# Optimization experiments

Measured on AMD Instinct MI355X. Metric: run time of the kernel, lower is better.

The kernel has to match this reference:

```python
import jax, jax.numpy as jnp
import numpy as np

H = 8           # attention heads
SPARSITY = 0.5  # fraction of keys kept per query row

def _silu(x):
    return x * jax.nn.sigmoid(x)

def _forward(x_t, t, te_w1, te_b1, te_w2, te_b2, fe_w1, fe_b1, fe_w2, fe_b2,
             fp_w1, fp_b1, fp_w2, fp_b2, fp_w3, fp_b3, fid_emb,
             wq, bq, wk, bk, wv, bv, wo, bo,
             gp_w1, gp_b1, gp_w2, gp_b2, ln_g, ln_b,
             dn_w1, dn_b1, dn_w2, dn_b2, dn_w3, dn_b3):
    B, F = x_t.shape
    D = te_w1.shape[1]
    hd = D // H
    # time / feature embeddings (Linear-SiLU-Linear)
    t_emb = _silu(t[:, None] @ te_w1 + te_b1) @ te_w2 + te_b2        # [B, D]
    x_emb = _silu(x_t @ fe_w1 + fe_b1) @ fe_w2 + fe_b2               # [B, D]
    comb = jnp.concatenate([
        jnp.broadcast_to(x_emb[:, None, :], (B, F, D)),
        jnp.broadcast_to(t_emb[:, None, :], (B, F, D))], axis=-1)    # [B, F, 2D]
    # shared per-feature processor (n_features > 32 branch)
    h = _silu(comb @ fp_w1 + fp_b1)
    h = _silu(h @ fp_w2 + fp_b2)
    h = h @ fp_w3 + fp_b3                                            # [B, F, D]
    d4 = fid_emb.shape[1]
    fid_pad = jnp.concatenate([fid_emb, jnp.zeros((F, D - d4), h.dtype)], axis=-1)
    feats = h + 0.1 * fid_pad[None]                                  # [B, F, D]
    # sparse feature attention (dropout is identity in eval)
    def split(x):
        return x.reshape(B, F, H, hd).transpose(0, 2, 1, 3)          # [B, H, F, hd]
    q = split(feats @ wq + bq)
    k = split(feats @ wk + bk)
    v = split(feats @ wv + bv)
    scores = jnp.einsum('bhqd,bhkd->bhqk', q, k) / (hd ** 0.5)
    k_value = max(1, int(F * SPARSITY))
    thr = jax.lax.top_k(scores, k_value)[0][..., -1:]                # kth largest per row
    scores = jnp.where(scores < thr, -1e9, scores)                   # masked_fill(-1e9)
    attn = jax.nn.softmax(scores, axis=-1)
    out = jnp.einsum('bhqk,bhkd->bhqd', attn, v)
    out = out.transpose(0, 2, 1, 3).reshape(B, F, D) @ wo + bo       # [B, F, D]
    # global pooling + processor with LayerNorm (eps=1e-5)
    g = out.mean(axis=1)
    g = _silu(g @ gp_w1 + gp_b1) @ gp_w2 + gp_b2
    mu = g.mean(-1, keepdims=True)
    var = ((g - mu) ** 2).mean(-1, keepdims=True)
    g = (g - mu) / jnp.sqrt(var + 1e-5) * ln_g + ln_b
    # denoise net -> tanh of mean half
    r = _silu(g @ dn_w1 + dn_b1)
    r = _silu(r @ dn_w2 + dn_b2)
    r = r @ dn_w3 + dn_b3                                            # [B, 2F]
    return jnp.tanh(r[:, :F])

def setup_inputs():
    B, F, D = 512, 128, 512
    D4 = D // 4
    ks = iter(jax.random.split(jax.random.key(0), 40))
    def w(shape):
        return jax.random.normal(next(ks), shape, jnp.float32) / np.sqrt(shape[0]).astype(np.float32)
    z = lambda n: jnp.zeros((n,), jnp.float32)
    return dict(
        x_t=jax.random.normal(next(ks), (B, F), jnp.float32),
        t=jax.random.uniform(next(ks), (B,), jnp.float32),
        te_w1=w((1, D)), te_b1=z(D), te_w2=w((D, D)), te_b2=z(D),
        fe_w1=w((F, D)), fe_b1=z(D), fe_w2=w((D, D)), fe_b2=z(D),
        fp_w1=w((2 * D, D)), fp_b1=z(D), fp_w2=w((D, D)), fp_b2=z(D),
        fp_w3=w((D, D)), fp_b3=z(D),
        fid_emb=jax.random.normal(next(ks), (F, D4), jnp.float32),
        wq=w((D, D)), bq=z(D), wk=w((D, D)), bk=z(D),
        wv=w((D, D)), bv=z(D), wo=w((D, D)), bo=z(D),
        gp_w1=w((D, 2 * D)), gp_b1=z(2 * D), gp_w2=w((2 * D, D)), gp_b2=z(D),
        ln_g=jnp.ones((D,), jnp.float32), ln_b=z(D),
        dn_w1=w((D, 2 * D)), dn_b1=z(2 * D), dn_w2=w((2 * D, 2 * D)), dn_b2=z(2 * D),
        dn_w3=w((2 * D, 2 * F)), dn_b3=z(2 * F),
    )

def reference(x_t, t, te_w1, te_b1, te_w2, te_b2, fe_w1, fe_b1, fe_w2, fe_b2,
              fp_w1, fp_b1, fp_w2, fp_b2, fp_w3, fp_b3, fid_emb,
              wq, bq, wk, bk, wv, bv, wo, bo,
              gp_w1, gp_b1, gp_w2, gp_b2, ln_g, ln_b,
              dn_w1, dn_b1, dn_w2, dn_b2, dn_w3, dn_b3):
    return _forward(x_t, t, te_w1, te_b1, te_w2, te_b2, fe_w1, fe_b1, fe_w2, fe_b2,
                    fp_w1, fp_b1, fp_w2, fp_b2, fp_w3, fp_b3, fid_emb,
                    wq, bq, wk, bk, wv, bv, wo, bo,
                    gp_w1, gp_b1, gp_w2, gp_b2, ln_g, ln_b,
                    dn_w1, dn_b1, dn_w2, dn_b2, dn_w3, dn_b3)
```

## Files before the change

kernel.cpp:

```cpp
#include <hip/hip_runtime.h>

__device__ __forceinline__ float silu_f(float x) { return x / (1.f + __expf(-x)); }

struct AOp {
  const float* P;
  const float* w1;
  const float* b0;
  int lda;
  int tgen;
};

template <int NPROB, int T1GEN>
__global__ __launch_bounds__(256) void gemm_p(
    AOp a0, AOp a1,
    const float* __restrict__ B0, const float* __restrict__ B1,
    const float* __restrict__ B2, int ldb,
    float* __restrict__ O0, float* __restrict__ O1, float* __restrict__ O2,
    int ldc, int Kslab, int ls, long slabMN) {
  __shared__ float As[2][32][68];
  __shared__ float Bs[2][32][68];
  const int tid = threadIdx.x;
  const int z = blockIdx.z;
  const int zi = (NPROB > 1) ? (z >> ls) : 0;
  const int s  = (NPROB > 1) ? (z & ((1 << ls) - 1)) : z;
  const AOp a = (NPROB > 1 && zi == 1) ? a1 : a0;
  const float* Bp = ((NPROB > 2 && zi == 2) ? B2 : (zi == 1) ? B1 : B0)
                    + (long)(s * Kslab) * ldb;
  float* Obase = ((NPROB > 2 && zi == 2) ? O2 : (zi == 1) ? O1 : O0)
                 + (long)s * slabMN;
  const int kbase = s * Kslab;
  const long bm = blockIdx.y * 64, bn = blockIdx.x * 64;
  const int tg = T1GEN ? a.tgen : 0;

  float acc[4][4] = {};
  const int ar = tid >> 3;
  const int ak = (tid & 7) << 2;
  const int br = tid >> 4;
  const int bn4 = (tid & 15) << 2;
  const int ty = tid >> 4, tx = tid & 15;

  float4 rA[2];
  float4 rB[2];
  float4 rW, rC;
  float tm0 = 0.f, tm1 = 0.f;

  auto loadA = [&](int k0) {
    int kg = kbase + k0 + ak;
    if (T1GEN && tg) {
      rW = *(const float4*)&a.w1[kg];
      rC = *(const float4*)&a.b0[kg];
    } else {
#pragma unroll
      for (int h = 0; h < 2; ++h)
        rA[h] = *(const float4*)&a.P[(bm + ar + h * 32) * (long)a.lda + kg];
    }
  };
  auto loadB = [&](int k0) {
#pragma unroll
    for (int h = 0; h < 2; ++h)
      rB[h] = *(const float4*)&Bp[(long)(k0 + br + h * 16) * ldb + bn + bn4];
  };
  auto store = [&](int buf) {
#pragma unroll
    for (int h = 0; h < 2; ++h) {
      int m = ar + h * 32;
      float4 av;
      if (T1GEN && tg) {
        float tm = h ? tm1 : tm0;
        av.x = silu_f(tm * rW.x + rC.x);
        av.y = silu_f(tm * rW.y + rC.y);
        av.z = silu_f(tm * rW.z + rC.z);
        av.w = silu_f(tm * rW.w + rC.w);
      } else {
        av = rA[h];
      }
      As[buf][ak + 0][m] = av.x; As[buf][ak + 1][m] = av.y;
      As[buf][ak + 2][m] = av.z; As[buf][ak + 3][m] = av.w;
    }
#pragma unroll
    for (int h = 0; h < 2; ++h) *(float4*)&Bs[buf][br + h * 16][bn4] = rB[h];
  };

  if (T1GEN && tg) { tm0 = a.P[bm + ar]; tm1 = a.P[bm + ar + 32]; }
  loadA(0); loadB(0);
  store(0);
  if (32 < Kslab) { loadA(32); loadB(32); }

  int cur = 0;
  for (int k0 = 0; k0 < Kslab; k0 += 32) {
    __syncthreads();
    if (k0 + 32 < Kslab) store(cur ^ 1);
    if (k0 + 64 < Kslab) { loadA(k0 + 64); loadB(k0 + 64); }
#pragma unroll
    for (int k = 0; k < 32; ++k) {
      float4 a4 = *(const float4*)&As[cur][k][ty << 2];
      float4 b4 = *(const float4*)&Bs[cur][k][tx << 2];
      float am[4] = {a4.x, a4.y, a4.z, a4.w};
      float bv[4] = {b4.x, b4.y, b4.z, b4.w};
#pragma unroll
      for (int i = 0; i < 4; ++i)
#pragma unroll
        for (int j = 0; j < 4; ++j) acc[i][j] = fmaf(am[i], bv[j], acc[i][j]);
    }
    cur ^= 1;
  }

  float* O = Obase + (bm + ty * 4) * (long)ldc + bn + tx * 4;
#pragma unroll
  for (int i = 0; i < 4; ++i) {
    float4 v = {acc[i][0], acc[i][1], acc[i][2], acc[i][3]};
    *(float4*)&O[(long)i * ldc] = v;
  }
}

__global__ __launch_bounds__(256) void gemm_bt(
    const float* __restrict__ A, int lda, const float* __restrict__ B, int ldb,
    float* __restrict__ OUT, int ldc, int K, float alpha,
    int zAoff, int zBoff, int zCoff) {
  __shared__ float As[2][32][68];
  __shared__ float Bs[2][32][68];
  const int tid = threadIdx.x;
  const int z = blockIdx.z;
  const long bm = blockIdx.y * 64, bn = blockIdx.x * 64;
  const float* Ab = A + (long)z * zAoff;
  const float* Bp = B + (long)z * zBoff;
  float* Obase = OUT + (long)z * zCoff;
  float acc[4][4] = {};
  const int ar = tid >> 3;
  const int ak = (tid & 7) << 2;
  const int ty = tid >> 4, tx = tid & 15;
  float4 rA[2], rB[2];
  auto loadAB = [&](int k0) {
#pragma unroll
    for (int h = 0; h < 2; ++h) {
      rA[h] = *(const float4*)&Ab[(bm + ar + h * 32) * (long)lda + k0 + ak];
      rB[h] = *(const float4*)&Bp[(bn + ar + h * 32) * (long)ldb + k0 + ak];
    }
  };
  auto store = [&](int buf) {
#pragma unroll
    for (int h = 0; h < 2; ++h) {
      int m = ar + h * 32;
      As[buf][ak + 0][m] = rA[h].x; As[buf][ak + 1][m] = rA[h].y;
      As[buf][ak + 2][m] = rA[h].z; As[buf][ak + 3][m] = rA[h].w;
      Bs[buf][ak + 0][m] = rB[h].x; Bs[buf][ak + 1][m] = rB[h].y;
      Bs[buf][ak + 2][m] = rB[h].z; Bs[buf][ak + 3][m] = rB[h].w;
    }
  };
  loadAB(0); store(0);
  if (32 < K) loadAB(32);
  int cur = 0;
  for (int k0 = 0; k0 < K; k0 += 32) {
    __syncthreads();
    if (k0 + 32 < K) store(cur ^ 1);
    if (k0 + 64 < K) loadAB(k0 + 64);
#pragma unroll
    for (int k = 0; k < 32; ++k) {
      float4 a4 = *(const float4*)&As[cur][k][ty << 2];
      float4 b4 = *(const float4*)&Bs[cur][k][tx << 2];
      float am[4] = {a4.x, a4.y, a4.z, a4.w};
      float bv[4] = {b4.x, b4.y, b4.z, b4.w};
#pragma unroll
      for (int i = 0; i < 4; ++i)
#pragma unroll
        for (int j = 0; j < 4; ++j) acc[i][j] = fmaf(am[i], bv[j], acc[i][j]);
    }
    cur ^= 1;
  }
  float* O = Obase + (bm + ty * 4) * (long)ldc + bn + tx * 4;
#pragma unroll
  for (int i = 0; i < 4; ++i) {
    float4 v = {alpha * acc[i][0], alpha * acc[i][1], alpha * acc[i][2],
                alpha * acc[i][3]};
    *(float4*)&O[(long)i * ldc] = v;
  }
}

template <int NS, int ACT>
__global__ __launch_bounds__(256) void sumk(
    const float* __restrict__ P, long slabMN,
    const float* __restrict__ b0, const float* __restrict__ b1, int bsplit,
    int cmask, float* __restrict__ out) {
  int i4 = (blockIdx.x * 256 + threadIdx.x) << 2;
  float4 s = *(const float4*)&P[i4];
#pragma unroll
  for (int si = 1; si < NS; ++si) {
    float4 p = *(const float4*)&P[(long)si * slabMN + i4];
    s.x += p.x; s.y += p.y; s.z += p.z; s.w += p.w;
  }
  int c = i4 & cmask;
  const float* bp = (b1 && c >= bsplit) ? (b1 + c - bsplit) : (b0 + c);
  float4 bb = *(const float4*)bp;
  s.x += bb.x; s.y += bb.y; s.z += bb.z; s.w += bb.w;
  if (ACT == 1) {
    s.x = silu_f(s.x); s.y = silu_f(s.y); s.z = silu_f(s.z); s.w = silu_f(s.w);
  }
  *(float4*)&out[i4] = s;
}

__global__ __launch_bounds__(256) void reduce_tanh(
    const float* __restrict__ P, int slabMN, int nslab,
    const float* __restrict__ bias, float* __restrict__ C) {
  int i4 = (blockIdx.x * 256 + threadIdx.x) << 2;
  float4 s = *(const float4*)&P[i4];
  for (int si = 1; si < nslab; ++si) {
    float4 p = *(const float4*)&P[(long)si * slabMN + i4];
    s.x += p.x; s.y += p.y; s.z += p.z; s.w += p.w;
  }
  int c = i4 & 127;
  float4 v = {tanhf(s.x + bias[c]), tanhf(s.y + bias[c + 1]),
              tanhf(s.z + bias[c + 2]), tanhf(s.w + bias[c + 3])};
  *(float4*)&C[i4] = v;
}

__global__ __launch_bounds__(256) void attn_kernel(
    const float* __restrict__ PBq,
    const float* __restrict__ bq,
    const float* __restrict__ bv,
    const float* __restrict__ kf,
    const float* __restrict__ Mm,
    const float* __restrict__ vf,
    float* __restrict__ pool) {
  const int b = blockIdx.x, h = blockIdx.y;
  const int tid = threadIdx.x;
  __shared__ float uq[64];
  __shared__ float uls[128];
  __shared__ float wpart[4][128];
  __shared__ float wcol[128];
  __shared__ float ppart[2][64];

  if (tid < 64) {
    int c = h * 64 + tid;
    long o = (long)b * 512 + c;
    uq[tid] = PBq[o] + PBq[262144 + o] + PBq[524288 + o] + PBq[786432 + o] + bq[c];
  }
  __syncthreads();
  if (tid < 128) {
    const float* kr = kf + (long)tid * 512 + h * 64;
    float acc = 0.f;
#pragma unroll
    for (int d4 = 0; d4 < 16; ++d4) {
      float4 kv = *(const float4*)&kr[d4 * 4];
      acc += uq[d4 * 4] * kv.x + uq[d4 * 4 + 1] * kv.y +
             uq[d4 * 4 + 2] * kv.z + uq[d4 * 4 + 3] * kv.w;
    }
    uls[tid] = 0.0125f * acc;
  }
  __syncthreads();

  const int lane = tid & 63;
  const int wave = tid >> 6;
  const float u0 = uls[lane], u1 = uls[lane + 64];

  float blo = -0.5f, bhi = 0.5f;
#pragma unroll
  for (int it = 0; it < 11; ++it) {
    float mid = 0.5f * (blo + bhi);
    int n = __popcll(__ballot(u0 >= mid)) + __popcll(__ballot(u1 >= mid));
    bool ge = (n >= 64);
    blo = ge ? mid : blo;
    bhi = ge ? bhi : mid;
  }
  const float wlo = blo - 0.014f, whi = blo + 0.014f;

  float wc0 = 0.f, wc1 = 0.f;
  const float* Mh = Mm + h * 128;
  const int i0 = wave * 32;
  float a0r = Mh[(long)i0 * 1024 + lane];
  float a1r = Mh[(long)i0 * 1024 + lane + 64];
  float b0r = Mh[(long)(i0 + 1) * 1024 + lane];
  float b1r = Mh[(long)(i0 + 1) * 1024 + lane + 64];
  for (int r = 0; r < 32; r += 2) {
    float TA0 = u0 + a0r, TA1 = u1 + a1r;
    float TB0 = u0 + b0r, TB1 = u1 + b1r;
    if (r < 30) {
      a0r = Mh[(long)(i0 + r + 2) * 1024 + lane];
      a1r = Mh[(long)(i0 + r + 2) * 1024 + lane + 64];
      b0r = Mh[(long)(i0 + r + 3) * 1024 + lane];
      b1r = Mh[(long)(i0 + r + 3) * 1024 + lane + 64];
    }
    float loA = wlo, hiA = whi, loB = wlo, hiB = whi;
#pragma unroll
    for (int it = 0; it < 5; ++it) {
      float midA = 0.5f * (loA + hiA), midB = 0.5f * (loB + hiB);
      int nA = __popcll(__ballot(TA0 >= midA)) + __popcll(__ballot(TA1 >= midA));
      int nB = __popcll(__ballot(TB0 >= midB)) + __popcll(__ballot(TB1 >= midB));
      bool gA = (nA >= 64), gB = (nB >= 64);
      loA = gA ? midA : loA; hiA = gA ? hiA : midA;
      loB = gB ? midB : loB; hiB = gB ? hiB : midB;
    }
    float pA0 = (TA0 >= loA) ? __expf(TA0 - loA) : 0.f;
    float pA1 = (TA1 >= loA) ? __expf(TA1 - loA) : 0.f;
    float pB0 = (TB0 >= loB) ? __expf(TB0 - loB) : 0.f;
    float pB1 = (TB1 >= loB) ? __expf(TB1 - loB) : 0.f;
    float sA = pA0 + pA1, sB = pB0 + pB1;
#pragma unroll
    for (int d = 1; d < 64; d <<= 1) {
      sA += __shfl_xor(sA, d);
      sB += __shfl_xor(sB, d);
    }
    float ivA = 1.f / sA, ivB = 1.f / sB;
    wc0 += pA0 * ivA + pB0 * ivB;
    wc1 += pA1 * ivA + pB1 * ivB;
  }
  wpart[wave][lane] = wc0;
  wpart[wave][lane + 64] = wc1;
  __syncthreads();
  if (tid < 128) {
    wcol[tid] = (wpart[0][tid] + wpart[1][tid] + wpart[2][tid] + wpart[3][tid]) *
                (1.f / 128.f);
  }
  __syncthreads();
  if (wave < 2) {
    int j0 = wave * 64;
    const float* vfp = vf + h * 64 + lane;
    float acc = 0.f;
#pragma unroll 8
    for (int jj = 0; jj < 64; ++jj) acc += wcol[j0 + jj] * vfp[(long)(j0 + jj) * 512];
    ppart[wave][lane] = acc;
  }
  __syncthreads();
  if (tid < 64) {
    int d = tid;
    int c = h * 64 + d;
    long o = (long)b * 512 + c;
    long vb0 = 4 * 262144;
    float v = PBq[vb0 + o] + PBq[vb0 + 262144 + o] + PBq[vb0 + 524288 + o] +
              PBq[vb0 + 786432 + o] + bv[c];
    pool[o] = 0.1f * (ppart[0][d] + ppart[1][d]) + v;
  }
}

template <int NSLAB>
__global__ __launch_bounds__(256) void ln_kernel(const float* __restrict__ P,
                                                 const float* __restrict__ bias,
                                                 const float* __restrict__ g,
                                                 const float* __restrict__ bb,
                                                 float* __restrict__ Y) {
  int row = blockIdx.x;
  int tid = threadIdx.x;
  long o0 = (long)row * 512 + tid;
  long o1 = o0 + 256;
  float v0 = bias[tid], v1 = bias[tid + 256];
#pragma unroll
  for (int s = 0; s < NSLAB; ++s) {
    v0 += P[(long)s * 262144 + o0];
    v1 += P[(long)s * 262144 + o1];
  }
  float s = v0 + v1;
#pragma unroll
  for (int d = 1; d < 64; d <<= 1) s += __shfl_xor(s, d);
  __shared__ float r1[4], r2[4];
  if ((tid & 63) == 0) r1[tid >> 6] = s;
  __syncthreads();
  float mean = (r1[0] + r1[1] + r1[2] + r1[3]) * (1.f / 512.f);
  float d0 = v0 - mean, d1 = v1 - mean;
  float q = d0 * d0 + d1 * d1;
#pragma unroll
  for (int d = 1; d < 64; d <<= 1) q += __shfl_xor(q, d);
  if ((tid & 63) == 0) r2[tid >> 6] = q;
  __syncthreads();
  float var = (r2[0] + r2[1] + r2[2] + r2[3]) * (1.f / 512.f);
  float inv = rsqrtf(var + 1e-5f);
  Y[(long)row * 512 + tid] = d0 * inv * g[tid] + bb[tid];
  Y[(long)row * 512 + tid + 256] = d1 * inv * g[tid + 256] + bb[tid + 256];
}


extern "C" void kernel_launch(void* const* d_in, const int* in_sizes, int n_in,
                              void* d_out, int out_size, void* d_ws, size_t ws_size,
                              hipStream_t stream) {
  const float* x_t = (const float*)d_in[0];
  const float* t_in = (const float*)d_in[1];
  const float* te_w1 = (const float*)d_in[2];
  const float* te_b1 = (const float*)d_in[3];
  const float* te_w2 = (const float*)d_in[4];
  const float* te_b2 = (const float*)d_in[5];
  const float* fe_w1 = (const float*)d_in[6];
  const float* fe_b1 = (const float*)d_in[7];
  const float* fe_w2 = (const float*)d_in[8];
  const float* fe_b2 = (const float*)d_in[9];
  const float* fp_w1 = (const float*)d_in[10];
  const float* fp_b1 = (const float*)d_in[11];
  const float* fp_w2 = (const float*)d_in[12];
  const float* fp_b2 = (const float*)d_in[13];
  const float* fp_w3 = (const float*)d_in[14];
  const float* fp_b3 = (const float*)d_in[15];
  const float* fid = (const float*)d_in[16];
  const float* wq = (const float*)d_in[17];
  const float* bq = (const float*)d_in[18];
  const float* wk = (const float*)d_in[19];
  const float* wv = (const float*)d_in[21];
  const float* bv = (const float*)d_in[22];
  const float* wo = (const float*)d_in[23];
  const float* bo = (const float*)d_in[24];
  const float* gp_w1 = (const float*)d_in[25];
  const float* gp_b1 = (const float*)d_in[26];
  const float* gp_w2 = (const float*)d_in[27];
  const float* gp_b2 = (const float*)d_in[28];
  const float* ln_g = (const float*)d_in[29];
  const float* ln_b = (const float*)d_in[30];
  const float* dn_w1 = (const float*)d_in[31];
  const float* dn_b1 = (const float*)d_in[32];
  const float* dn_w2 = (const float*)d_in[33];
  const float* dn_b2 = (const float*)d_in[34];
  const float* dn_w3 = (const float*)d_in[35];
  const float* dn_b3 = (const float*)d_in[36];

  float* W = (float*)d_ws;
  float* P  = W;
  float* XC = W + 2097152;
  float* SA = W + 2621440;
  float* SB = W + 2883584;
  float* qf = W + 3145728;
  float* kf = W + 3211264;
  float* vf = W + 3276800;
  float* Mb = W + 3342336;

  auto ap = [](const float* Pm, int lda) {
    AOp a; a.P = Pm; a.w1 = nullptr; a.b0 = nullptr; a.lda = lda; a.tgen = 0;
    return a;
  };

  gemm_p<3, 0><<<dim3(8, 2, 3), 256, 0, stream>>>(
      ap(fid, 128), ap(fid, 128), wq, wk, wv, 512, qf, kf, vf, 512, 128, 0, 0);
  gemm_bt<<<dim3(2, 2, 8), 256, 0, stream>>>(qf, 512, kf, 512, Mb, 1024, 64,
                                             0.00125f, 64, 64, 128);
  gemm_p<1, 0><<<dim3(8, 8, 4), 256, 0, stream>>>(
      ap(x_t, 128), ap(x_t, 128), fe_w1, nullptr, nullptr, 512,
      P, nullptr, nullptr, 512, 32, 0, 262144);
  sumk<4, 1><<<256, 256, 0, stream>>>(P, 262144, fe_b1, nullptr, 0, 511, SA);
  {
    AOp a1; a1.P = t_in; a1.w1 = te_w1; a1.b0 = te_b1; a1.lda = 0; a1.tgen = 1;
    gemm_p<2, 1><<<dim3(8, 8, 8), 256, 0, stream>>>(
        ap(SA, 512), a1, fe_w2, te_w2, nullptr, 512,
        P, P + 512, nullptr, 1024, 128, 2, 524288);
  }
  sumk<4, 0><<<512, 256, 0, stream>>>(P, 524288, fe_b2, te_b2, 512, 1023, XC);
  gemm_p<1, 0><<<dim3(8, 8, 8), 256, 0, stream>>>(
      ap(XC, 1024), ap(XC, 1024), fp_w1, nullptr, nullptr, 512,
      P, nullptr, nullptr, 512, 128, 0, 262144);
  sumk<8, 1><<<256, 256, 0, stream>>>(P, 262144, fp_b1, nullptr, 0, 511, SB);
  gemm_p<1, 0><<<dim3(8, 8, 8), 256, 0, stream>>>(
      ap(SB, 512), ap(SB, 512), fp_w2, nullptr, nullptr, 512,
      P, nullptr, nullptr, 512, 64, 0, 262144);
  sumk<8, 1><<<256, 256, 0, stream>>>(P, 262144, fp_b2, nullptr, 0, 511, SA);
  gemm_p<1, 0><<<dim3(8, 8, 8), 256, 0, stream>>>(
      ap(SA, 512), ap(SA, 512), fp_w3, nullptr, nullptr, 512,
      P, nullptr, nullptr, 512, 64, 0, 262144);
  sumk<8, 0><<<256, 256, 0, stream>>>(P, 262144, fp_b3, nullptr, 0, 511, SB);
  gemm_p<2, 0><<<dim3(8, 8, 8), 256, 0, stream>>>(
      ap(SB, 512), ap(SB, 512), wq, wv, nullptr, 512,
      P, P + 1048576, nullptr, 512, 128, 2, 262144);
  attn_kernel<<<dim3(512, 8), 256, 0, stream>>>(P, bq, bv, kf, Mb, vf, SA);
  gemm_p<1, 0><<<dim3(8, 8, 8), 256, 0, stream>>>(
      ap(SA, 512), ap(SA, 512), wo, nullptr, nullptr, 512,
      P, nullptr, nullptr, 512, 64, 0, 262144);
  sumk<8, 0><<<256, 256, 0, stream>>>(P, 262144, bo, nullptr, 0, 511, SB);
  gemm_p<1, 0><<<dim3(16, 8, 4), 256, 0, stream>>>(
      ap(SB, 512), ap(SB, 512), gp_w1, nullptr, nullptr, 1024,
      P, nullptr, nullptr, 1024, 128, 0, 524288);
  sumk<4, 1><<<512, 256, 0, stream>>>(P, 524288, gp_b1, nullptr, 0, 1023, XC);
  gemm_p<1, 0><<<dim3(8, 8, 8), 256, 0, stream>>>(
      ap(XC, 1024), ap(XC, 1024), gp_w2, nullptr, nullptr, 512,
      P, nullptr, nullptr, 512, 128, 0, 262144);
  ln_kernel<8><<<512, 256, 0, stream>>>(P, gp_b2, ln_g, ln_b, SA);
  gemm_p<1, 0><<<dim3(16, 8, 4), 256, 0, stream>>>(
      ap(SA, 512), ap(SA, 512), dn_w1, nullptr, nullptr, 1024,
      P, nullptr, nullptr, 1024, 128, 0, 524288);
  sumk<4, 1><<<512, 256, 0, stream>>>(P, 524288, dn_b1, nullptr, 0, 1023, XC);
  gemm_p<1, 0><<<dim3(16, 8, 4), 256, 0, stream>>>(
      ap(XC, 1024), ap(XC, 1024), dn_w2, nullptr, nullptr, 1024,
      P, nullptr, nullptr, 1024, 256, 0, 524288);
  sumk<4, 1><<<512, 256, 0, stream>>>(P, 524288, dn_b2, nullptr, 0, 1023, XC);
  gemm_p<1, 0><<<dim3(2, 8, 16), 256, 0, stream>>>(
      ap(XC, 1024), ap(XC, 1024), dn_w3, nullptr, nullptr, 256,
      P, nullptr, nullptr, 128, 64, 0, 65536);
  reduce_tanh<<<64, 256, 0, stream>>>(P, 65536, 16, dn_b3, (float*)d_out);
}
```

Baseline: 288.0 us.

## Fuse split-K reductions into GEMMs via atomic tile counters and prefold fp_w1 weights

Split-K partial sums are now reduced inside the GEMM kernel by the last-arriving block for each tile, tracked with an atomic counter, which replaces the separate sumk and reduce_tanh launches. The fe_w2/te_w2 products with fp_w1 are precomputed as weight-weight GEMMs, and a folded bias is built, so the concatenated 1024-wide embedding step collapses into one GEMM per branch. Several small prologue GEMMs (QKV of fid, QK^T mask, first feature layer) are merged into two multi-role kernels. This cuts launch count and intermediate traffic, at the cost of threadfence/atomic overhead, a memset, and some extra weight-weight GEMM work per call.

```diff
diff --git a/kernel.cpp b/kernel.cpp
--- a/kernel.cpp
+++ b/kernel.cpp
@@ -2,70 +2,50 @@
 
 __device__ __forceinline__ float silu_f(float x) { return x / (1.f + __expf(-x)); }
 
-struct AOp {
-  const float* P;
-  const float* w1;
-  const float* b0;
-  int lda;
-  int tgen;
-};
-
-template <int NPROB, int T1GEN>
-__global__ __launch_bounds__(256) void gemm_p(
-    AOp a0, AOp a1,
-    const float* __restrict__ B0, const float* __restrict__ B1,
-    const float* __restrict__ B2, int ldb,
-    float* __restrict__ O0, float* __restrict__ O1, float* __restrict__ O2,
-    int ldc, int Kslab, int ls, long slabMN) {
-  __shared__ float As[2][32][68];
-  __shared__ float Bs[2][32][68];
+template <int TG, int BT>
+__device__ __forceinline__ void dev_gemm(
+    float (*As)[32][68], float (*Bs)[32][68],
+    const float* __restrict__ Ap, int lda,
+    const float* __restrict__ tw1, const float* __restrict__ tb0,
+    const float* __restrict__ Bp, int ldb,
+    float* __restrict__ Obase, int ldc,
+    int kbase, int Kslab, long bm, long bn, float alpha) {
   const int tid = threadIdx.x;
-  const int z = blockIdx.z;
-  const int zi = (NPROB > 1) ? (z >> ls) : 0;
-  const int s  = (NPROB > 1) ? (z & ((1 << ls) - 1)) : z;
-  const AOp a = (NPROB > 1 && zi == 1) ? a1 : a0;
-  const float* Bp = ((NPROB > 2 && zi == 2) ? B2 : (zi == 1) ? B1 : B0)
-                    + (long)(s * Kslab) * ldb;
-  float* Obase = ((NPROB > 2 && zi == 2) ? O2 : (zi == 1) ? O1 : O0)
-                 + (long)s * slabMN;
-  const int kbase = s * Kslab;
-  const long bm = blockIdx.y * 64, bn = blockIdx.x * 64;
-  const int tg = T1GEN ? a.tgen : 0;
-
+  const int ar = tid >> 3, ak = (tid & 7) << 2;
+  const int br = tid >> 4, bn4 = (tid & 15) << 2;
+  const int ty = tid >> 4, tx = tid & 15;
   float acc[4][4] = {};
-  const int ar = tid >> 3;
-  const int ak = (tid & 7) << 2;
-  const int br = tid >> 4;
-  const int bn4 = (tid & 15) << 2;
-  const int ty = tid >> 4, tx = tid & 15;
-
-  float4 rA[2];
-  float4 rB[2];
-  float4 rW, rC;
+  float4 rA[2], rB[2], rW, rC;
   float tm0 = 0.f, tm1 = 0.f;
-
+  if (TG) { tm0 = Ap[bm + ar]; tm1 = Ap[bm + ar + 32]; }
   auto loadA = [&](int k0) {
     int kg = kbase + k0 + ak;
-    if (T1GEN && tg) {
-      rW = *(const float4*)&a.w1[kg];
-      rC = *(const float4*)&a.b0[kg];
+    if (TG) {
+      rW = *(const float4*)&tw1[kg];
+      rC = *(const float4*)&tb0[kg];
     } else {
 #pragma unroll
       for (int h = 0; h < 2; ++h)
-        rA[h] = *(const float4*)&a.P[(bm + ar + h * 32) * (long)a.lda + kg];
+        rA[h] = *(const float4*)&Ap[(bm + ar + h * 32) * (long)lda + kg];
     }
   };
   auto loadB = [&](int k0) {
-#pragma unroll
-    for (int h = 0; h < 2; ++h)
-      rB[h] = *(const float4*)&Bp[(long)(k0 + br + h * 16) * ldb + bn + bn4];
+    if (BT) {
+#pragma unroll
+      for (int h = 0; h < 2; ++h)
+        rB[h] = *(const float4*)&Bp[(bn + ar + h * 32) * (long)ldb + kbase + k0 + ak];
+    } else {
+#pragma unroll
+      for (int h = 0; h < 2; ++h)
+        rB[h] = *(const float4*)&Bp[(long)(k0 + br + h * 16) * ldb + bn + bn4];
+    }
   };
   auto store = [&](int buf) {
 #pragma unroll
     for (int h = 0; h < 2; ++h) {
       int m = ar + h * 32;
       float4 av;
-      if (T1GEN && tg) {
+      if (TG) {
         float tm = h ? tm1 : tm0;
         av.x = silu_f(tm * rW.x + rC.x);
         av.y = silu_f(tm * rW.y + rC.y);
@@ -77,15 +57,21 @@
       As[buf][ak + 0][m] = av.x; As[buf][ak + 1][m] = av.y;
       As[buf][ak + 2][m] = av.z; As[buf][ak + 3][m] = av.w;
     }
-#pragma unroll
-    for (int h = 0; h < 2; ++h) *(float4*)&Bs[buf][br + h * 16][bn4] = rB[h];
+    if (BT) {
+#pragma unroll
+      for (int h = 0; h < 2; ++h) {
+        int n = ar + h * 32;
+        Bs[buf][ak + 0][n] = rB[h].x; Bs[buf][ak + 1][n] = rB[h].y;
+        Bs[buf][ak + 2][n] = rB[h].z; Bs[buf][ak + 3][n] = rB[h].w;
+      }
+    } else {
+#pragma unroll
+      for (int h = 0; h < 2; ++h) *(float4*)&Bs[buf][br + h * 16][bn4] = rB[h];
+    }
   };
-
-  if (T1GEN && tg) { tm0 = a.P[bm + ar]; tm1 = a.P[bm + ar + 32]; }
   loadA(0); loadB(0);
   store(0);
   if (32 < Kslab) { loadA(32); loadB(32); }
-
   int cur = 0;
   for (int k0 = 0; k0 < Kslab; k0 += 32) {
     __syncthreads();
@@ -104,69 +90,6 @@
     }
     cur ^= 1;
   }
-
-  float* O = Obase + (bm + ty * 4) * (long)ldc + bn + tx * 4;
-#pragma unroll
-  for (int i = 0; i < 4; ++i) {
-    float4 v = {acc[i][0], acc[i][1], acc[i][2], acc[i][3]};
-    *(float4*)&O[(long)i * ldc] = v;
-  }
-}
-
-__global__ __launch_bounds__(256) void gemm_bt(
-    const float* __restrict__ A, int lda, const float* __restrict__ B, int ldb,
-    float* __restrict__ OUT, int ldc, int K, float alpha,
-    int zAoff, int zBoff, int zCoff) {
-  __shared__ float As[2][32][68];
-  __shared__ float Bs[2][32][68];
-  const int tid = threadIdx.x;
-  const int z = blockIdx.z;
-  const long bm = blockIdx.y * 64, bn = blockIdx.x * 64;
-  const float* Ab = A + (long)z * zAoff;
-  const float* Bp = B + (long)z * zBoff;
-  float* Obase = OUT + (long)z * zCoff;
-  float acc[4][4] = {};
-  const int ar = tid >> 3;
-  const int ak = (tid & 7) << 2;
-  const int ty = tid >> 4, tx = tid & 15;
-  float4 rA[2], rB[2];
-  auto loadAB = [&](int k0) {
-#pragma unroll
-    for (int h = 0; h < 2; ++h) {
-      rA[h] = *(const float4*)&Ab[(bm + ar + h * 32) * (long)lda + k0 + ak];
-      rB[h] = *(const float4*)&Bp[(bn + ar + h * 32) * (long)ldb + k0 + ak];
-    }
-  };
-  auto store = [&](int buf) {
-#pragma unroll
-    for (int h = 0; h < 2; ++h) {
-      int m = ar + h * 32;
-      As[buf][ak + 0][m] = rA[h].x; As[buf][ak + 1][m] = rA[h].y;
-      As[buf][ak + 2][m] = rA[h].z; As[buf][ak + 3][m] = rA[h].w;
-      Bs[buf][ak + 0][m] = rB[h].x; Bs[buf][ak + 1][m] = rB[h].y;
-      Bs[buf][ak + 2][m] = rB[h].z; Bs[buf][ak + 3][m] = rB[h].w;
-    }
-  };
-  loadAB(0); store(0);
-  if (32 < K) loadAB(32);
-  int cur = 0;
-  for (int k0 = 0; k0 < K; k0 += 32) {
-    __syncthreads();
-    if (k0 + 32 < K) store(cur ^ 1);
-    if (k0 + 64 < K) loadAB(k0 + 64);
-#pragma unroll
-    for (int k = 0; k < 32; ++k) {
-      float4 a4 = *(const float4*)&As[cur][k][ty << 2];
-      float4 b4 = *(const float4*)&Bs[cur][k][tx << 2];
-      float am[4] = {a4.x, a4.y, a4.z, a4.w};
-      float bv[4] = {b4.x, b4.y, b4.z, b4.w};
-#pragma unroll
-      for (int i = 0; i < 4; ++i)
-#pragma unroll
-        for (int j = 0; j < 4; ++j) acc[i][j] = fmaf(am[i], bv[j], acc[i][j]);
-    }
-    cur ^= 1;
-  }
   float* O = Obase + (bm + ty * 4) * (long)ldc + bn + tx * 4;
 #pragma unroll
   for (int i = 0; i < 4; ++i) {
@@ -176,50 +99,139 @@
   }
 }
 
-template <int NS, int ACT>
-__global__ __launch_bounds__(256) void sumk(
-    const float* __restrict__ P, long slabMN,
-    const float* __restrict__ b0, const float* __restrict__ b1, int bsplit,
-    int cmask, float* __restrict__ out) {
-  int i4 = (blockIdx.x * 256 + threadIdx.x) << 2;
-  float4 s = *(const float4*)&P[i4];
-#pragma unroll
-  for (int si = 1; si < NS; ++si) {
-    float4 p = *(const float4*)&P[(long)si * slabMN + i4];
-    s.x += p.x; s.y += p.y; s.z += p.z; s.w += p.w;
-  }
-  int c = i4 & cmask;
-  const float* bp = (b1 && c >= bsplit) ? (b1 + c - bsplit) : (b0 + c);
-  float4 bb = *(const float4*)bp;
-  s.x += bb.x; s.y += bb.y; s.z += bb.z; s.w += bb.w;
-  if (ACT == 1) {
-    s.x = silu_f(s.x); s.y = silu_f(s.y); s.z = silu_f(s.z); s.w = silu_f(s.w);
-  }
-  *(float4*)&out[i4] = s;
-}
-
-__global__ __launch_bounds__(256) void reduce_tanh(
-    const float* __restrict__ P, int slabMN, int nslab,
-    const float* __restrict__ bias, float* __restrict__ C) {
-  int i4 = (blockIdx.x * 256 + threadIdx.x) << 2;
-  float4 s = *(const float4*)&P[i4];
-  for (int si = 1; si < nslab; ++si) {
-    float4 p = *(const float4*)&P[(long)si * slabMN + i4];
-    s.x += p.x; s.y += p.y; s.z += p.z; s.w += p.w;
-  }
-  int c = i4 & 127;
-  float4 v = {tanhf(s.x + bias[c]), tanhf(s.y + bias[c + 1]),
-              tanhf(s.z + bias[c + 2]), tanhf(s.w + bias[c + 3])};
-  *(float4*)&C[i4] = v;
+template <int RACT>
+__device__ __forceinline__ void reduce_tile(
+    const float* __restrict__ Pb, long slabMN, int nslab,
+    const float* __restrict__ bias, float* __restrict__ cmp, int ldcmp,
+    long bm, long bn, int ldc) {
+  const int tid = threadIdx.x;
+  const int r0 = (tid >> 4) * 4, c0 = (tid & 15) * 4;
+  float4 bb = *(const float4*)&bias[bn + c0];
+#pragma unroll
+  for (int i = 0; i < 4; ++i) {
+    long off = (bm + r0 + i) * (long)ldc + bn + c0;
+    float4 s = *(const float4*)&Pb[off];
+    for (int sl = 1; sl < nslab; ++sl) {
+      float4 p = *(const float4*)&Pb[(long)sl * slabMN + off];
+      s.x += p.x; s.y += p.y; s.z += p.z; s.w += p.w;
+    }
+    s.x += bb.x; s.y += bb.y; s.z += bb.z; s.w += bb.w;
+    if (RACT == 1) {
+      s.x = silu_f(s.x); s.y = silu_f(s.y); s.z = silu_f(s.z); s.w = silu_f(s.w);
+    }
+    if (RACT == 2) {
+      s.x = tanhf(s.x); s.y = tanhf(s.y); s.z = tanhf(s.z); s.w = tanhf(s.w);
+    }
+    *(float4*)&cmp[(bm + r0 + i) * (long)ldcmp + bn + c0] = s;
+  }
+}
+
+template <int NPROB, int T1GEN, int RACT>
+__global__ __launch_bounds__(256) void gemm_f(
+    const float* A0, const float* A1, const float* tw1, const float* tb0,
+    int lda, const float* B0, const float* B1, int ldb,
+    float* Parena, int ldc, long slabMN, int Kslab, int ls,
+    unsigned* cnt, float* cmp, int ldcmp, const float* bias, int nslab) {
+  __shared__ float As[2][32][68];
+  __shared__ float Bs[2][32][68];
+  __shared__ unsigned sflag;
+  const int z = blockIdx.z;
+  const int zi = (NPROB > 1) ? (z >> ls) : 0;
+  const int s = (NPROB > 1) ? (z & ((1 << ls) - 1)) : z;
+  const int kbase = s * Kslab;
+  const long bm = blockIdx.y * 64, bn = blockIdx.x * 64;
+  const float* Bsel = zi ? B1 : B0;
+  const float* Bp = Bsel + (long)kbase * ldb;
+  float* Obase = Parena + (long)((zi << ls) + s) * slabMN;
+  if (T1GEN && zi == 1)
+    dev_gemm<1, 0>(As, Bs, A1, 0, tw1, tb0, Bp, ldb, Obase, ldc, kbase, Kslab,
+                   bm, bn, 1.f);
+  else
+    dev_gemm<0, 0>(As, Bs, zi ? A1 : A0, lda, nullptr, nullptr, Bp, ldb, Obase,
+                   ldc, kbase, Kslab, bm, bn, 1.f);
+  if (RACT >= 0) {
+    __threadfence();
+    __syncthreads();
+    if (threadIdx.x == 0) {
+      int tileId = blockIdx.y * gridDim.x + blockIdx.x;
+      sflag = atomicAdd(&cnt[tileId], 1u);
+    }
+    __syncthreads();
+    if (sflag == (unsigned)(nslab - 1)) {
+      __threadfence();
+      reduce_tile<RACT>(Parena, slabMN, nslab, bias, cmp, ldcmp, bm, bn, ldc);
+    }
+  }
+}
+
+__global__ __launch_bounds__(256) void pre1(
+    const float* fid, const float* wq, const float* wk, const float* wv,
+    const float* x_t, const float* fe_w1, const float* fe_b1,
+    const float* fe_w2, const float* te_w2, const float* fp_w1,
+    float* qf, float* kf, float* vf, float* P, float* SA, float* Wx, float* Wt,
+    unsigned* cntA) {
+  __shared__ float As[2][32][68];
+  __shared__ float Bs[2][32][68];
+  __shared__ unsigned sflag;
+  const int w = blockIdx.x;
+  if (w < 48) {
+    int prob = w >> 4, t = w & 15;
+    const float* B = prob == 0 ? wq : (prob == 1 ? wk : wv);
+    float* O = prob == 0 ? qf : (prob == 1 ? kf : vf);
+    dev_gemm<0, 0>(As, Bs, fid, 128, nullptr, nullptr, B, 512, O, 512, 0, 128,
+                   (t >> 3) * 64, (t & 7) * 64, 1.f);
+  } else if (w < 304) {
+    int w2 = w - 48, s = w2 & 3, t = w2 >> 2;
+    long bm = (t >> 3) * 64, bn = (t & 7) * 64;
+    dev_gemm<0, 0>(As, Bs, x_t, 128, nullptr, nullptr,
+                   fe_w1 + (long)(s * 32) * 512, 512, P + (long)s * 262144, 512,
+                   s * 32, 32, bm, bn, 1.f);
+    __threadfence();
+    __syncthreads();
+    if (threadIdx.x == 0) sflag = atomicAdd(&cntA[t], 1u);
+    __syncthreads();
+    if (sflag == 3u) {
+      __threadfence();
+      reduce_tile<1>(P, 262144, 4, fe_b1, SA, 512, bm, bn, 512);
+    }
+  } else if (w < 368) {
+    int t = w - 304;
+    dev_gemm<0, 0>(As, Bs, fe_w2, 512, nullptr, nullptr, fp_w1, 512, Wx, 512,
+                   0, 512, (t >> 3) * 64, (t & 7) * 64, 1.f);
+  } else {
+    int t = w - 368;
+    dev_gemm<0, 0>(As, Bs, te_w2, 512, nullptr, nullptr, fp_w1 + 512 * 512, 512,
+                   Wt, 512, 0, 512, (t >> 3) * 64, (t & 7) * 64, 1.f);
+  }
+}
+
+__global__ __launch_bounds__(256) void pre2(
+    const float* qf, const float* kf, float* Mb,
+    const float* fp_b1, const float* fe_b2, const float* te_b2,
+    const float* fp_w1, float* beff1) {
+  __shared__ float As[2][32][68];
+  __shared__ float Bs[2][32][68];
+  const int w = blockIdx.x;
+  if (w < 32) {
+    int h = w >> 2, t = w & 3;
+    dev_gemm<0, 1>(As, Bs, qf + h * 64, 512, nullptr, nullptr, kf + h * 64, 512,
+                   Mb + h * 128, 1024, 0, 64, (t >> 1) * 64, (t & 1) * 64,
+                   0.00125f);
+  } else {
+    int c = (w - 32) * 256 + threadIdx.x;
+    float acc = fp_b1[c];
+    for (int k = 0; k < 512; ++k) {
+      acc += fe_b2[k] * fp_w1[(long)k * 512 + c];
+      acc += te_b2[k] * fp_w1[(long)(512 + k) * 512 + c];
+    }
+    beff1[c] = acc;
+  }
 }
 
 __global__ __launch_bounds__(256) void attn_kernel(
-    const float* __restrict__ PBq,
-    const float* __restrict__ bq,
-    const float* __restrict__ bv,
-    const float* __restrict__ kf,
-    const float* __restrict__ Mm,
-    const float* __restrict__ vf,
+    const float* __restrict__ PBq, const float* __restrict__ bq,
+    const float* __restrict__ bv, const float* __restrict__ kf,
+    const float* __restrict__ Mm, const float* __restrict__ vf,
     float* __restrict__ pool) {
   const int b = blockIdx.x, h = blockIdx.y;
   const int tid = threadIdx.x;
@@ -331,7 +343,6 @@
   }
 }
 
-template <int NSLAB>
 __global__ __launch_bounds__(256) void ln_kernel(const float* __restrict__ P,
                                                  const float* __restrict__ bias,
                                                  const float* __restrict__ g,
@@ -343,7 +354,7 @@
   long o1 = o0 + 256;
   float v0 = bias[tid], v1 = bias[tid + 256];
 #pragma unroll
-  for (int s = 0; s < NSLAB; ++s) {
+  for (int s = 0; s < 8; ++s) {
     v0 += P[(long)s * 262144 + o0];
     v1 += P[(long)s * 262144 + o1];
   }
@@ -365,7 +376,6 @@
   Y[(long)row * 512 + tid] = d0 * inv * g[tid] + bb[tid];
   Y[(long)row * 512 + tid + 256] = d1 * inv * g[tid + 256] + bb[tid + 256];
 }
-
 
 extern "C" void kernel_launch(void* const* d_in, const int* in_sizes, int n_in,
                               void* d_out, int out_size, void* d_ws, size_t ws_size,
@@ -408,73 +418,66 @@
   const float* dn_b3 = (const float*)d_in[36];
 
   float* W = (float*)d_ws;
-  float* P  = W;
-  float* XC = W + 2097152;
-  float* SA = W + 2621440;
-  float* SB = W + 2883584;
-  float* qf = W + 3145728;
-  float* kf = W + 3211264;
-  float* vf = W + 3276800;
-  float* Mb = W + 3342336;
-
-  auto ap = [](const float* Pm, int lda) {
-    AOp a; a.P = Pm; a.w1 = nullptr; a.b0 = nullptr; a.lda = lda; a.tgen = 0;
-    return a;
-  };
-
-  gemm_p<3, 0><<<dim3(8, 2, 3), 256, 0, stream>>>(
-      ap(fid, 128), ap(fid, 128), wq, wk, wv, 512, qf, kf, vf, 512, 128, 0, 0);
-  gemm_bt<<<dim3(2, 2, 8), 256, 0, stream>>>(qf, 512, kf, 512, Mb, 1024, 64,
-                                             0.00125f, 64, 64, 128);
-  gemm_p<1, 0><<<dim3(8, 8, 4), 256, 0, stream>>>(
-      ap(x_t, 128), ap(x_t, 128), fe_w1, nullptr, nullptr, 512,
-      P, nullptr, nullptr, 512, 32, 0, 262144);
-  sumk<4, 1><<<256, 256, 0, stream>>>(P, 262144, fe_b1, nullptr, 0, 511, SA);
-  {
-    AOp a1; a1.P = t_in; a1.w1 = te_w1; a1.b0 = te_b1; a1.lda = 0; a1.tgen = 1;
-    gemm_p<2, 1><<<dim3(8, 8, 8), 256, 0, stream>>>(
-        ap(SA, 512), a1, fe_w2, te_w2, nullptr, 512,
-        P, P + 512, nullptr, 1024, 128, 2, 524288);
-  }
-  sumk<4, 0><<<512, 256, 0, stream>>>(P, 524288, fe_b2, te_b2, 512, 1023, XC);
-  gemm_p<1, 0><<<dim3(8, 8, 8), 256, 0, stream>>>(
-      ap(XC, 1024), ap(XC, 1024), fp_w1, nullptr, nullptr, 512,
-      P, nullptr, nullptr, 512, 128, 0, 262144);
-  sumk<8, 1><<<256, 256, 0, stream>>>(P, 262144, fp_b1, nullptr, 0, 511, SB);
-  gemm_p<1, 0><<<dim3(8, 8, 8), 256, 0, stream>>>(
-      ap(SB, 512), ap(SB, 512), fp_w2, nullptr, nullptr, 512,
-      P, nullptr, nullptr, 512, 64, 0, 262144);
-  sumk<8, 1><<<256, 256, 0, stream>>>(P, 262144, fp_b2, nullptr, 0, 511, SA);
-  gemm_p<1, 0><<<dim3(8, 8, 8), 256, 0, stream>>>(
-      ap(SA, 512), ap(SA, 512), fp_w3, nullptr, nullptr, 512,
-      P, nullptr, nullptr, 512, 64, 0, 262144);
-  sumk<8, 0><<<256, 256, 0, stream>>>(P, 262144, fp_b3, nullptr, 0, 511, SB);
-  gemm_p<2, 0><<<dim3(8, 8, 8), 256, 0, stream>>>(
-      ap(SB, 512), ap(SB, 512), wq, wv, nullptr, 512,
-      P, P + 1048576, nullptr, 512, 128, 2, 262144);
-  attn_kernel<<<dim3(512, 8), 256, 0, stream>>>(P, bq, bv, kf, Mb, vf, SA);
-  gemm_p<1, 0><<<dim3(8, 8, 8), 256, 0, stream>>>(
-      ap(SA, 512), ap(SA, 512), wo, nullptr, nullptr, 512,
-      P, nullptr, nullptr, 512, 64, 0, 262144);
-  sumk<8, 0><<<256, 256, 0, stream>>>(P, 262144, bo, nullptr, 0, 511, SB);
-  gemm_p<1, 0><<<dim3(16, 8, 4), 256, 0, stream>>>(
-      ap(SB, 512), ap(SB, 512), gp_w1, nullptr, nullptr, 1024,
-      P, nullptr, nullptr, 1024, 128, 0, 524288);
-  sumk<4, 1><<<512, 256, 0, stream>>>(P, 524288, gp_b1, nullptr, 0, 1023, XC);
-  gemm_p<1, 0><<<dim3(8, 8, 8), 256, 0, stream>>>(
-      ap(XC, 1024), ap(XC, 1024), gp_w2, nullptr, nullptr, 512,
-      P, nullptr, nullptr, 512, 128, 0, 262144);
-  ln_kernel<8><<<512, 256, 0, stream>>>(P, gp_b2, ln_g, ln_b, SA);
-  gemm_p<1, 0><<<dim3(16, 8, 4), 256, 0, stream>>>(
-      ap(SA, 512), ap(SA, 512), dn_w1, nullptr, nullptr, 1024,
-      P, nullptr, nullptr, 1024, 128, 0, 524288);
-  sumk<4, 1><<<512, 256, 0, stream>>>(P, 524288, dn_b1, nullptr, 0, 1023, XC);
-  gemm_p<1, 0><<<dim3(16, 8, 4), 256, 0, stream>>>(
-      ap(XC, 1024), ap(XC, 1024), dn_w2, nullptr, nullptr, 1024,
-      P, nullptr, nullptr, 1024, 256, 0, 524288);
-  sumk<4, 1><<<512, 256, 0, stream>>>(P, 524288, dn_b2, nullptr, 0, 1023, XC);
-  gemm_p<1, 0><<<dim3(2, 8, 16), 256, 0, stream>>>(
-      ap(XC, 1024), ap(XC, 1024), dn_w3, nullptr, nullptr, 256,
-      P, nullptr, nullptr, 128, 64, 0, 65536);
-  reduce_tanh<<<64, 256, 0, stream>>>(P, 65536, 16, dn_b3, (float*)d_out);
-}
+  float* P   = W;
+  float* XC  = W + 2097152;
+  float* SB  = W + 2621440;
+  float* SC  = W + 2883584;
+  float* XC2 = SB;
+  float* SA  = W + 3145728;
+  float* Wx  = W + 3407872;
+  float* Wt  = W + 3670016;
+  float* qf  = W + 3932160;
+  float* kf  = W + 3997696;
+  float* vf  = W + 4063232;
+  float* Mb  = W + 4128768;
+  float* beff1 = W + 4259840;
+  unsigned* cnt = (unsigned*)(W + 4260864);
+
+  unsigned* cA  = cnt;
+  unsigned* cH1 = cnt + 64;
+  unsigned* cH2 = cnt + 128;
+  unsigned* cB  = cnt + 192;
+  unsigned* cG1 = cnt + 256;
+  unsigned* cG2 = cnt + 320;
+  unsigned* cR1 = cnt + 448;
+  unsigned* cR2 = cnt + 576;
+  unsigned* cO  = cnt + 704;
+
+  hipMemsetAsync(cnt, 0, 4096, stream);
+
+  pre1<<<432, 256, 0, stream>>>(fid, wq, wk, wv, x_t, fe_w1, fe_b1, fe_w2,
+                                te_w2, fp_w1, qf, kf, vf, P, SA, Wx, Wt, cA);
+  pre2<<<34, 256, 0, stream>>>(qf, kf, Mb, fp_b1, fe_b2, te_b2, fp_w1, beff1);
+  gemm_f<2, 1, 1><<<dim3(8, 8, 8), 256, 0, stream>>>(
+      SA, t_in, te_w1, te_b1, 512, Wx, Wt, 512, P, 512, 262144, 128, 2,
+      cH1, SB, 512, beff1, 8);
+  gemm_f<1, 0, 1><<<dim3(8, 8, 8), 256, 0, stream>>>(
+      SB, nullptr, nullptr, nullptr, 512, fp_w2, nullptr, 512, P, 512, 262144,
+      64, 0, cH2, SC, 512, fp_b2, 8);
+  gemm_f<1, 0, 0><<<dim3(8, 8, 8), 256, 0, stream>>>(
+      SC, nullptr, nullptr, nullptr, 512, fp_w3, nullptr, 512, P, 512, 262144,
+      64, 0, cB, SA, 512, fp_b3, 8);
+  gemm_f<2, 0, -1><<<dim3(8, 8, 8), 256, 0, stream>>>(
+      SA, SA, nullptr, nullptr, 512, wq, wv, 512, P, 512, 262144, 128, 2,
+      nullptr, nullptr, 0, nullptr, 0);
+  attn_kernel<<<dim3(512, 8), 256, 0, stream>>>(P, bq, bv, kf, Mb, vf, SB);
+  gemm_f<1, 0, 0><<<dim3(8, 8, 8), 256, 0, stream>>>(
+      SB, nullptr, nullptr, nullptr, 512, wo, nullptr, 512, P, 512, 262144,
+      64, 0, cG1, SC, 512, bo, 8);
+  gemm_f<1, 0, 1><<<dim3(16, 8, 4), 256, 0, stream>>>(
+      SC, nullptr, nullptr, nullptr, 512, gp_w1, nullptr, 1024, P, 1024, 524288,
+      128, 0, cG2, XC, 1024, gp_b1, 4);
+  gemm_f<1, 0, -1><<<dim3(8, 8, 8), 256, 0, stream>>>(
+      XC, nullptr, nullptr, nullptr, 1024, gp_w2, nullptr, 512, P, 512, 262144,
+      128, 0, nullptr, nullptr, 0, nullptr, 0);
+  ln_kernel<<<512, 256, 0, stream>>>(P, gp_b2, ln_g, ln_b, SA);
+  gemm_f<1, 0, 1><<<dim3(16, 8, 4), 256, 0, stream>>>(
+      SA, nullptr, nullptr, nullptr, 512, dn_w1, nullptr, 1024, P, 1024, 524288,
+      128, 0, cR1, XC, 1024, dn_b1, 4);
+  gemm_f<1, 0, 1><<<dim3(16, 8, 4), 256, 0, stream>>>(
+      XC, nullptr, nullptr, nullptr, 1024, dn_w2, nullptr, 1024, P, 1024, 524288,
+      256, 0, cR2, XC2, 1024, dn_b2, 4);
+  gemm_f<1, 0, 2><<<dim3(2, 8, 16), 256, 0, stream>>>(
+      XC2, nullptr, nullptr, nullptr, 1024, dn_w3, nullptr, 256, P, 128, 65536,
+      64, 0, cO, (float*)d_out, 128, dn_b3, 16);
+}
```

Result: slower. 843.8 us (+193.0%).
